# Performance work log

Hardware: AMD Instinct MI355X
Metric: run time of the kernel (lower is better)

Reference implementation:

```python
import jax, jax.numpy as jnp
import numpy as np

# Static configuration (matches init_kwargs)
B, C, H, W = 8, 64, 256, 256
WS = 8            # window size
HEADS = 4
DH = 16           # dim per head, HEADS*DH == C
L = WS * WS       # tokens per window
EPS_LN = 1e-5

# --- Swin relative-position index (static, numpy) ---
_coords = np.stack(np.meshgrid(np.arange(WS), np.arange(WS), indexing='ij'))  # [2,ws,ws]
_flat = _coords.reshape(2, -1)                                                # [2,L]
_rel = (_flat[:, :, None] - _flat[:, None, :]).transpose(1, 2, 0).copy()      # [L,L,2]
_rel[..., 0] += WS - 1
_rel[..., 1] += WS - 1
_rel[..., 0] *= 2 * WS - 1
REL_IDX = _rel.sum(-1)  # [L,L] ints in [0, (2ws-1)^2)


def _biasfree_ln(x, w):
    # x: [B,C,H,W]; BiasFree_LayerNorm over channel dim (biased var, no mean subtraction in scale)
    var = jnp.var(x, axis=1, keepdims=True)
    return x * jax.lax.rsqrt(var + EPS_LN) * w[None, :, None, None]


def _win_partition(t):  # [B,H,W,C] -> [N, L, C]
    t = t.reshape(B, H // WS, WS, W // WS, WS, C).transpose(0, 1, 3, 2, 4, 5)
    return t.reshape(-1, L, C)


def _win_reverse(t):  # [N, L, C] -> [B,H,W,C]
    t = t.reshape(B, H // WS, W // WS, WS, WS, C).transpose(0, 1, 3, 2, 4, 5)
    return t.reshape(B, H, W, C)


def _l2norm(t):
    # torch F.normalize(dim=-1) semantics
    n = jnp.sqrt(jnp.sum(t * t, axis=-1, keepdims=True))
    return t / jnp.maximum(n, 1e-12)


def _forward(x, illu_fea, ln1_w, ln2_w, w_qkv, b_qkv, rpb_table, w_proj, b_proj,
             temperature, w_qkv_m, w_dw, w_out_m):
    # ---------- spatial (window) attention branch ----------
    xs = _biasfree_ln(x, ln1_w).transpose(0, 2, 3, 1)          # [B,H,W,C]
    xw = _win_partition(xs)                                     # [N,L,C]
    iw = _win_partition(illu_fea.transpose(0, 2, 3, 1))         # [N,L,C]
    iw = iw.reshape(-1, L, HEADS, DH).transpose(0, 2, 1, 3)     # [N,h,L,d]

    qkv = (xw @ w_qkv + b_qkv).reshape(-1, L, 3, HEADS, DH).transpose(2, 0, 3, 1, 4)
    q, k, v = qkv[0], qkv[1], qkv[2]                            # [N,h,L,d]
    scale = DH ** (-0.5)
    attn = jnp.einsum('nhld,nhmd->nhlm', q * scale, k)          # [N,h,L,L]
    bias = rpb_table[REL_IDX.reshape(-1)].reshape(L, L, HEADS).transpose(2, 0, 1)
    attn = jax.nn.softmax(attn + bias[None], axis=-1)
    v = v * iw                                                  # illumination modulation
    out = jnp.einsum('nhlm,nhmd->nhld', attn, v)
    out = out.transpose(0, 2, 1, 3).reshape(-1, L, C) @ w_proj + b_proj
    win_out = _win_reverse(out).transpose(0, 3, 1, 2)           # [B,C,H,W]

    # ---------- channel (MDTA) attention branch ----------
    xm = _biasfree_ln(x, ln2_w)
    qkv_m = jnp.einsum('oc,bchw->bohw', w_qkv_m, xm)            # 1x1 conv, [B,3C,H,W]
    qkv_m = jax.lax.conv_general_dilated(
        qkv_m, w_dw, (1, 1), 'SAME', feature_group_count=3 * C,
        dimension_numbers=('NCHW', 'OIHW', 'NCHW'))             # depthwise 3x3
    qm, km, vm = jnp.split(qkv_m, 3, axis=1)                    # [B,C,H,W] each

    def heads(t):
        return t.reshape(B, HEADS, DH, H * W)                   # b (n d) h w -> b n d (hw)
    qm, km, vm, im = heads(qm), heads(km), heads(vm), heads(illu_fea)
    qm = _l2norm(qm)
    km = _l2norm(km)
    attn_c = jnp.einsum('bndx,bnex->bnde', qm, km) * temperature[None]  # [B,h,d,d]
    attn_c = jax.nn.softmax(attn_c, axis=-1)
    vm = vm * im                                                # illumination modulation
    out_c = jnp.einsum('bnde,bnex->bndx', attn_c, vm).reshape(B, C, H, W)
    mdta_out = jnp.einsum('oc,bchw->bohw', w_out_m, out_c)

    return x + win_out + mdta_out


def setup_inputs() -> dict:
    key = jax.random.key(0)
    ks = jax.random.split(key, 10)
    f32 = jnp.float32
    return {
        'x': jax.random.normal(ks[0], (B, C, H, W), f32),
        'illu_fea': jax.random.uniform(ks[1], (B, C, H, W), f32),
        'ln1_w': jnp.ones((C,), f32),
        'ln2_w': jnp.ones((C,), f32),
        'w_qkv': jax.random.normal(ks[2], (C, 3 * C), f32) * 0.02,
        'b_qkv': jnp.zeros((3 * C,), f32),
        'rpb_table': jax.random.normal(ks[3], ((2 * WS - 1) ** 2, HEADS), f32) * 0.02,
        'w_proj': jax.random.normal(ks[4], (C, C), f32) * 0.02,
        'b_proj': jnp.zeros((C,), f32),
        'temperature': jnp.ones((HEADS, 1, 1), f32),
        'w_qkv_m': jax.random.normal(ks[5], (3 * C, C), f32) * 0.02,
        'w_dw': jax.random.normal(ks[6], (3 * C, 1, 3, 3), f32) * 0.1,
        'w_out_m': jax.random.normal(ks[7], (C, C), f32) * 0.02,
    }


def reference(x, illu_fea, ln1_w, ln2_w, w_qkv, b_qkv, rpb_table, w_proj, b_proj,
              temperature, w_qkv_m, w_dw, w_out_m):
    return _forward(x, illu_fea, ln1_w, ln2_w, w_qkv, b_qkv, rpb_table, w_proj,
                    b_proj, temperature, w_qkv_m, w_dw, w_out_m)
```

## Files before the change

kernel.cpp:

```cpp
#include <hip/hip_runtime.h>
#include <hip/hip_bf16.h>

#define HW 65536
#define WIDTH 256
#define SP_OFF 77856768ull

typedef __attribute__((ext_vector_type(8))) short short8v;
typedef __attribute__((ext_vector_type(4))) short short4v;
typedef __attribute__((ext_vector_type(4))) float f32x4;

__device__ inline float bf2f(unsigned short u) {
  unsigned int i = ((unsigned int)u) << 16;
  float f; __builtin_memcpy(&f, &i, 4); return f;
}
__device__ inline unsigned short f2bf(float x) {
  __hip_bfloat16 h = __float2bfloat16(x);
  unsigned short u; __builtin_memcpy(&u, &h, 2); return u;
}

#define XH_IDX(p, g) ((p)*64 + ((((g) ^ ((p)&7)))<<3))
#define QC_IDX(ch, px) ((ch)*256 + ((((px)>>3) ^ ((ch)&7))<<3) + ((px)&7))
#define QCG_IDX(ch, G) ((ch)*256 + ((((G) ^ ((ch)&7)))<<3))

__global__ __launch_bounds__(256, 2) void k_spatial(
    const float* __restrict__ x, const float* __restrict__ illu,
    const float* __restrict__ ln1w, const float* __restrict__ wqkv,
    const float* __restrict__ bqkv, const float* __restrict__ rpb,
    const float* __restrict__ wproj, const float* __restrict__ bproj,
    float* __restrict__ out, unsigned short* __restrict__ sp, int use_sp)
{
  __shared__ __align__(16) unsigned short shbuf[9216];
  __shared__ __align__(16) unsigned short ks[64*72];
  __shared__ __align__(16) unsigned short vs[64*72];
  __shared__ __align__(16) unsigned short vsT[64*72];
  __shared__ __align__(16) unsigned short wq[192*72];
  __shared__ float rpbs[900];
  __shared__ float bq_s[192];
  __shared__ float rs_tok[64];

  unsigned short* xw = shbuf;
  unsigned short* qs = shbuf + 4608;

  const int tid = threadIdx.x;
  const int lb = ((blockIdx.x & 7) << 10) | (blockIdx.x >> 3);
  const int b = lb >> 10;
  const int win = lb & 1023;
  const int h0 = (win >> 5) << 3;
  const int w0 = (win & 31) << 3;
  const float* xb = x + (size_t)b * 64 * HW;

  const int lane = tid & 63;
  const int w = tid >> 6;
  const int fr = lane & 15;
  const int fg = lane >> 4;
  const int hb = w * 16;

  for (int i = tid; i < 900; i += 256) rpbs[i] = rpb[i];
  for (int i = tid; i < 192; i += 256) bq_s[i] = bqkv[i];
  for (int i = tid; i < 12288; i += 256) {
    int c = i / 192, o = i - c * 192;
    wq[o*72 + c] = f2bf(wqkv[i] * ln1w[c]);
  }
  for (int i = tid; i < 1024; i += 256) {
    int c = i >> 4, seg = i & 15;
    int row = seg >> 1, half = (seg & 1) * 4;
    float4 v4 = *(const float4*)&xb[(size_t)c * HW + (h0 + row) * WIDTH + w0 + half];
    int p = row * 8 + half;
    xw[(p+0)*72 + c] = f2bf(v4.x);
    xw[(p+1)*72 + c] = f2bf(v4.y);
    xw[(p+2)*72 + c] = f2bf(v4.z);
    xw[(p+3)*72 + c] = f2bf(v4.w);
  }
  __syncthreads();
  {
    int l = tid >> 2, q4 = tid & 3;
    short8v v8a = *(const short8v*)&xw[l*72 + q4*16];
    short8v v8b = *(const short8v*)&xw[l*72 + q4*16 + 8];
    float s = 0.f, s2 = 0.f;
    #pragma unroll
    for (int j = 0; j < 8; ++j) {
      float va = bf2f((unsigned short)v8a[j]), vb = bf2f((unsigned short)v8b[j]);
      s += va + vb; s2 += va * va + vb * vb;
    }
    s += __shfl_down(s, 1); s2 += __shfl_down(s2, 1);
    s += __shfl_down(s, 2); s2 += __shfl_down(s2, 2);
    if (q4 == 0) {
      float mean = s * 0.015625f;
      float var = s2 * 0.015625f - mean * mean;
      rs_tok[l] = rsqrtf(var + 1e-5f);
    }
  }
  __syncthreads();
  {
    short8v a[4][2];
    #pragma unroll
    for (int rt = 0; rt < 4; ++rt)
      #pragma unroll
      for (int kh = 0; kh < 2; ++kh)
        a[rt][kh] = *(const short8v*)&xw[(rt*16 + fr)*72 + kh*32 + fg*8];
    #pragma unroll
    for (int part = 0; part < 3; ++part) {
      int ob = part * 64 + hb;
      short8v b0 = *(const short8v*)&wq[(ob + fr)*72 + fg*8];
      short8v b1 = *(const short8v*)&wq[(ob + fr)*72 + 32 + fg*8];
      float bias = bq_s[ob + fr];
      #pragma unroll
      for (int rt = 0; rt < 4; ++rt) {
        f32x4 acc = {0.f, 0.f, 0.f, 0.f};
        acc = __builtin_amdgcn_mfma_f32_16x16x32_bf16(a[rt][0], b0, acc, 0, 0, 0);
        acc = __builtin_amdgcn_mfma_f32_16x16x32_bf16(a[rt][1], b1, acc, 0, 0, 0);
        #pragma unroll
        for (int r = 0; r < 4; ++r) {
          int t = rt*16 + fg*4 + r;
          float val = acc[r] * rs_tok[t] + bias;
          if (part == 0)      qs[t*72 + hb + fr] = f2bf(val * 0.25f);
          else if (part == 1) ks[t*72 + hb + fr] = f2bf(val);
          else                vs[t*72 + hb + fr] = f2bf(val);
        }
      }
    }
  }
  __syncthreads();
  {
    const float* ib = illu + (size_t)b * 64 * HW;
    for (int i = tid; i < 1024; i += 256) {
      int c = i >> 4, seg = i & 15;
      int row = seg >> 1, half = (seg & 1) * 4;
      float4 v4 = *(const float4*)&ib[(size_t)c * HW + (h0 + row) * WIDTH + w0 + half];
      int p = row * 8 + half;
      xw[(p+0)*72 + c] = f2bf(v4.x);
      xw[(p+1)*72 + c] = f2bf(v4.y);
      xw[(p+2)*72 + c] = f2bf(v4.z);
      xw[(p+3)*72 + c] = f2bf(v4.w);
    }
    for (int i = tid; i < 4096; i += 256) {
      int c = i >> 6, o = i & 63;
      wq[o*72 + c] = f2bf(wproj[i]);
    }
  }
  __syncthreads();
  for (int i = tid; i < 4096; i += 256) {
    int l = i >> 6, c = i & 63;
    unsigned short vb16 = f2bf(bf2f(vs[l*72 + c]) * bf2f(xw[l*72 + c]));
    vs[l*72 + c] = vb16;
    vsT[c*72 + ((((l >> 3) ^ (c & 7)) << 3) | (l & 7))] = vb16;
  }
  __syncthreads();
  float inv_s[4];
  {
    short8v zero8 = {0,0,0,0,0,0,0,0};
    short8v kf[4], qf[4];
    #pragma unroll
    for (int t = 0; t < 4; ++t) {
      if (fg < 2) {
        kf[t] = *(const short8v*)&ks[(t*16 + fr)*72 + hb + fg*8];
        qf[t] = *(const short8v*)&qs[(t*16 + fr)*72 + hb + fg*8];
      } else { kf[t] = zero8; qf[t] = zero8; }
    }
    f32x4 st[4][4];
    #pragma unroll
    for (int kt = 0; kt < 4; ++kt)
      #pragma unroll
      for (int qt = 0; qt < 4; ++qt) {
        f32x4 z = {0.f, 0.f, 0.f, 0.f};
        st[kt][qt] = __builtin_amdgcn_mfma_f32_16x16x32_bf16(kf[kt], qf[qt], z, 0, 0, 0);
      }
    float sc[4][16];
    #pragma unroll
    for (int qt = 0; qt < 4; ++qt) {
      int qi = qt*2 + (fr >> 3);
      int qj = fr & 7;
      float mx = -1e30f;
      #pragma unroll
      for (int kt = 0; kt < 4; ++kt) {
        int ki = kt*2 + (fg >> 1);
        int kj0 = (fg & 1) * 4;
        int base = ((qi - ki + 7)*15 + (qj - kj0 + 7))*4 + w;
        #pragma unroll
        for (int r = 0; r < 4; ++r) {
          float v = st[kt][qt][r] + rpbs[base - 4*r];
          sc[qt][kt*4 + r] = v;
          mx = fmaxf(mx, v);
        }
      }
      mx = fmaxf(mx, __shfl_xor(mx, 16));
      mx = fmaxf(mx, __shfl_xor(mx, 32));
      float ss = 0.f;
      #pragma unroll
      for (int j = 0; j < 16; ++j) { float e = __expf(sc[qt][j] - mx); sc[qt][j] = e; ss += e; }
      ss += __shfl_xor(ss, 16);
      ss += __shfl_xor(ss, 32);
      inv_s[qt] = 1.f / ss;
    }
    __syncthreads();
    unsigned short* pb = shbuf + w * 2304;
    f32x4 ot[4];
    #pragma unroll
    for (int nt = 0; nt < 4; ++nt) { f32x4 z = {0.f,0.f,0.f,0.f}; ot[nt] = z; }
    #pragma unroll
    for (int P = 0; P < 2; ++P) {
      #pragma unroll
      for (int qt = 0; qt < 4; ++qt)
        #pragma unroll
        for (int k2 = 0; k2 < 2; ++k2) {
          int kt = 2*P + k2;
          unsigned int lo = (unsigned)f2bf(sc[qt][kt*4+0]) | ((unsigned)f2bf(sc[qt][kt*4+1]) << 16);
          unsigned int hi = (unsigned)f2bf(sc[qt][kt*4+2]) | ((unsigned)f2bf(sc[qt][kt*4+3]) << 16);
          uint2 pk; pk.x = lo; pk.y = hi;
          *(uint2*)&pb[(qt*16 + fr)*36 + k2*16 + fg*4] = pk;
        }
      __syncthreads();
      short8v av = *(const short8v*)&vsT[(hb + fr)*72 + (((P*4 + fg) ^ ((hb + fr) & 7)) << 3)];
      #pragma unroll
      for (int nt = 0; nt < 4; ++nt) {
        short4v p0 = *(const short4v*)&pb[(nt*16 + fr)*36 + fg*8];
        short4v p1 = *(const short4v*)&pb[(nt*16 + fr)*36 + fg*8 + 4];
        short8v bv;
        #pragma unroll
        for (int j = 0; j < 4; ++j) { bv[j] = p0[j]; bv[4+j] = p1[j]; }
        ot[nt] = __builtin_amdgcn_mfma_f32_16x16x32_bf16(av, bv, ot[nt], 0, 0, 0);
      }
      __syncthreads();
    }
    #pragma unroll
    for (int nt = 0; nt < 4; ++nt) {
      float iv = inv_s[nt];
      unsigned int lo = (unsigned)f2bf(ot[nt][0]*iv) | ((unsigned)f2bf(ot[nt][1]*iv) << 16);
      unsigned int hi = (unsigned)f2bf(ot[nt][2]*iv) | ((unsigned)f2bf(ot[nt][3]*iv) << 16);
      uint2 pk; pk.x = lo; pk.y = hi;
      *(uint2*)&ks[(nt*16 + fr)*72 + hb + fg*4] = pk;
    }
  }
  __syncthreads();
  {
    short8v a[4][2];
    #pragma unroll
    for (int rt = 0; rt < 4; ++rt)
      #pragma unroll
      for (int kh = 0; kh < 2; ++kh)
        a[rt][kh] = *(const short8v*)&ks[(rt*16 + fr)*72 + kh*32 + fg*8];
    short8v b0 = *(const short8v*)&wq[(hb + fr)*72 + fg*8];
    short8v b1 = *(const short8v*)&wq[(hb + fr)*72 + 32 + fg*8];
    #pragma unroll
    for (int rt = 0; rt < 4; ++rt) {
      f32x4 acc = {0.f, 0.f, 0.f, 0.f};
      acc = __builtin_amdgcn_mfma_f32_16x16x32_bf16(a[rt][0], b0, acc, 0, 0, 0);
      acc = __builtin_amdgcn_mfma_f32_16x16x32_bf16(a[rt][1], b1, acc, 0, 0, 0);
      #pragma unroll
      for (int r = 0; r < 4; ++r)
        vs[(rt*16 + fg*4 + r)*72 + hb + fr] = f2bf(acc[r]);
    }
  }
  __syncthreads();
  if (use_sp) {
    unsigned short* spw = sp + (size_t)(b * 1024 + win) * 4096;
    for (int i = tid; i < 1024; i += 256) {
      int row = i >> 7, rem = i & 127;
      int c = rem >> 1, half = (rem & 1) * 4;
      int p = row * 8 + half;
      size_t gofs = (size_t)c * HW + (h0 + row) * WIDTH + w0 + half;
      float4 xr4 = *(const float4*)&xb[gofs];
      float bp = bproj[c];
      unsigned int lo = (unsigned)f2bf(xr4.x + bp + bf2f(vs[(p+0)*72 + c]))
                      | ((unsigned)f2bf(xr4.y + bp + bf2f(vs[(p+1)*72 + c])) << 16);
      unsigned int hi = (unsigned)f2bf(xr4.z + bp + bf2f(vs[(p+2)*72 + c]))
                      | ((unsigned)f2bf(xr4.w + bp + bf2f(vs[(p+3)*72 + c])) << 16);
      uint2 pk; pk.x = lo; pk.y = hi;
      *(uint2*)&spw[row*512 + c*8 + half] = pk;
    }
  } else {
    for (int i = tid; i < 1024; i += 256) {
      int o = i >> 4, seg = i & 15;
      int row = seg >> 1, half = (seg & 1) * 4;
      int p = row * 8 + half;
      size_t gofs = (size_t)o * HW + (h0 + row) * WIDTH + w0 + half;
      float4 xr4 = *(const float4*)&xb[gofs];
      float bp = bproj[o];
      float4 r;
      r.x = xr4.x + bp + bf2f(vs[(p+0)*72 + o]);
      r.y = xr4.y + bp + bf2f(vs[(p+1)*72 + o]);
      r.z = xr4.z + bp + bf2f(vs[(p+2)*72 + o]);
      r.w = xr4.w + bp + bf2f(vs[(p+3)*72 + o]);
      *(float4*)&out[(size_t)b * 64 * HW + gofs] = r;
    }
  }
}

__global__ __launch_bounds__(256, 2) void k_chan_qkv(
    const float* __restrict__ x, const float* __restrict__ illu,
    const float* __restrict__ ln2w, const float* __restrict__ w1,
    const float* __restrict__ wdw,
    unsigned short* __restrict__ vm, float* __restrict__ Gp,
    float* __restrict__ Nqp, float* __restrict__ Nkp)
{
  __shared__ __align__(16) unsigned short xh[336*64];
  __shared__ __align__(16) unsigned short tb[16*360];
  __shared__ __align__(16) unsigned short qc[16*256];
  __shared__ __align__(16) unsigned short kc[16*256];
  __shared__ float rsp[324];

  const int tid = threadIdx.x;
  const int blk = blockIdx.x;
  const int b = blk >> 8;
  const int tile = blk & 255;
  const int ty0 = (tile >> 4) << 4, tx0 = (tile & 15) << 4;
  const float* xb = x + (size_t)b * 64 * HW;

  for (int i = tid; i < 64 * 324; i += 256) {
    int c = i / 324, p = i - c * 324;
    int hy = p / 18, hx = p - hy * 18;
    int gy = ty0 + hy - 1, gx = tx0 + hx - 1;
    float v = 0.f;
    if (gy >= 0 && gy < 256 && gx >= 0 && gx < 256)
      v = xb[(size_t)c * HW + gy * WIDTH + gx];
    xh[XH_IDX(p, c >> 3) + (c & 7)] = f2bf(v);
  }
  for (int i = tid; i < 12 * 64; i += 256) {
    int p = 324 + (i >> 6), c = i & 63;
    xh[XH_IDX(p, c >> 3) + (c & 7)] = 0;
  }
  __syncthreads();
  for (int p = tid; p < 324; p += 256) {
    float s = 0.f, s2 = 0.f;
    #pragma unroll
    for (int g = 0; g < 8; ++g) {
      short8v v8 = *(const short8v*)&xh[XH_IDX(p, g)];
      #pragma unroll
      for (int j = 0; j < 8; ++j) { float v = bf2f((unsigned short)v8[j]); s += v; s2 += v * v; }
    }
    float mean = s * 0.015625f;
    float var = s2 * 0.015625f - mean * mean;
    rsp[p] = rsqrtf(var + 1e-5f);
  }
  __syncthreads();

  const int lane = tid & 63;
  const int wid = tid >> 6;
  const int fcol = lane & 15;
  const int fk = lane >> 4;
  const int dpy = (tid >> 2) & 15;
  const int dg = tid & 3;

  auto gemm_chunk = [&](int wbase) {
    short8v bf[2];
    const float* wr = w1 + (size_t)(wbase + fcol) * 64;
    #pragma unroll
    for (int s = 0; s < 2; ++s) {
      int cs = fk * 8 + s * 32;
      #pragma unroll
      for (int j = 0; j < 8; ++j)
        bf[s][j] = (short)f2bf(wr[cs + j] * ln2w[cs + j]);
    }
    for (int t = wid; t < 21; t += 4) {
      int ar = t * 16 + fcol;
      short8v a0 = *(const short8v*)&xh[XH_IDX(ar, fk)];
      short8v a1 = *(const short8v*)&xh[XH_IDX(ar, fk + 4)];
      f32x4 acc = {0.f, 0.f, 0.f, 0.f};
      acc = __builtin_amdgcn_mfma_f32_16x16x32_bf16(a0, bf[0], acc, 0, 0, 0);
      acc = __builtin_amdgcn_mfma_f32_16x16x32_bf16(a1, bf[1], acc, 0, 0, 0);
      #pragma unroll
      for (int r = 0; r < 4; ++r) {
        int px = t * 16 + fk * 4 + r;
        if (px < 324) {
          int hy = px / 18, hx = px - hy * 18;
          tb[fcol * 360 + hy * 20 + hx] = f2bf(acc[r] * rsp[px]);
        }
      }
    }
  };

  float dout4[4][4];
  auto dw_chunk = [&](int wbase) {
    #pragma unroll
    for (int oc4 = 0; oc4 < 4; ++oc4) {
      int oc = wid * 4 + oc4;
      const float* w9 = wdw + (size_t)(wbase + oc) * 9;
      float wk[9];
      #pragma unroll
      for (int t = 0; t < 9; ++t) wk[t] = w9[t];
      float a0 = 0.f, a1 = 0.f, a2 = 0.f, a3 = 0.f;
      #pragma unroll
      for (int ky = 0; ky < 3; ++ky) {
        int base = oc * 360 + (dpy + ky) * 20 + dg * 4;
        short4v t4 = *(const short4v*)&tb[base];
        unsigned int t2 = *(const unsigned int*)&tb[base + 4];
        float e0 = bf2f((unsigned short)t4[0]);
        float e1 = bf2f((unsigned short)t4[1]);
        float e2 = bf2f((unsigned short)t4[2]);
        float e3 = bf2f((unsigned short)t4[3]);
        float e4 = bf2f((unsigned short)(t2 & 0xffff));
        float e5 = bf2f((unsigned short)(t2 >> 16));
        float k0 = wk[ky*3+0], k1 = wk[ky*3+1], k2 = wk[ky*3+2];
        a0 += k0*e0 + k1*e1 + k2*e2;
        a1 += k0*e1 + k1*e2 + k2*e3;
        a2 += k0*e2 + k1*e3 + k2*e4;
        a3 += k0*e3 + k1*e4 + k2*e5;
      }
      dout4[oc4][0] = a0; dout4[oc4][1] = a1;
      dout4[oc4][2] = a2; dout4[oc4][3] = a3;
    }
  };

  for (int n = 0; n < 4; ++n) {
    gemm_chunk(16 * n);
    __syncthreads();
    dw_chunk(16 * n);
    #pragma unroll
    for (int oc4 = 0; oc4 < 4; ++oc4)
      #pragma unroll
      for (int i = 0; i < 4; ++i)
        qc[QC_IDX(wid*4 + oc4, dpy*16 + dg*4 + i)] = f2bf(dout4[oc4][i]);
    __syncthreads();
    {
      int ch = tid >> 4, seg = tid & 15;
      float s = 0.f;
      #pragma unroll
      for (int j = 0; j < 16; ++j) { float v = bf2f(qc[QC_IDX(ch, seg * 16 + j)]); s += v * v; }
      s += __shfl_xor(s, 1); s += __shfl_xor(s, 2); s += __shfl_xor(s, 4); s += __shfl_xor(s, 8);
      if (seg == 0) Nqp[(size_t)blk * 64 + n * 16 + ch] = s;
    }
    gemm_chunk(64 + 16 * n);
    __syncthreads();
    dw_chunk(64 + 16 * n);
    #pragma unroll
    for (int oc4 = 0; oc4 < 4; ++oc4)
      #pragma unroll
      for (int i = 0; i < 4; ++i)
        kc[QC_IDX(wid*4 + oc4, dpy*16 + dg*4 + i)] = f2bf(dout4[oc4][i]);
    __syncthreads();
    {
      int ch = tid >> 4, seg = tid & 15;
      float s = 0.f;
      #pragma unroll
      for (int j = 0; j < 16; ++j) { float v = bf2f(kc[QC_IDX(ch, seg * 16 + j)]); s += v * v; }
      s += __shfl_xor(s, 1); s += __shfl_xor(s, 2); s += __shfl_xor(s, 4); s += __shfl_xor(s, 8);
      if (seg == 0) Nkp[(size_t)blk * 64 + n * 16 + ch] = s;
    }
    if (wid == 0) {
      f32x4 g = {0.f, 0.f, 0.f, 0.f};
      #pragma unroll
      for (int s = 0; s < 8; ++s) {
        int G = fk + 4 * s;
        short8v aq = *(const short8v*)&qc[QCG_IDX(fcol, G)];
        short8v bk = *(const short8v*)&kc[QCG_IDX(fcol, G)];
        g = __builtin_amdgcn_mfma_f32_16x16x32_bf16(aq, bk, g, 0, 0, 0);
      }
      float* gp = Gp + ((size_t)blk * 4 + n) * 256;
      #pragma unroll
      for (int r = 0; r < 4; ++r) gp[(fk * 4 + r) * 16 + fcol] = g[r];
    }
  }
  const float* ib = illu + (size_t)b * 64 * HW;
  for (int j = 0; j < 4; ++j) {
    gemm_chunk(128 + 16 * j);
    __syncthreads();
    dw_chunk(128 + 16 * j);
    int gy = ty0 + dpy, gx = tx0 + dg * 4;
    size_t ppos = (size_t)gy * WIDTH + gx;
    #pragma unroll
    for (int oc4 = 0; oc4 < 4; ++oc4) {
      int vc = 16 * j + wid * 4 + oc4;
      float4 iv4 = *(const float4*)&ib[(size_t)vc * HW + ppos];
      unsigned int lo = (unsigned)f2bf(dout4[oc4][0] * iv4.x)
                      | ((unsigned)f2bf(dout4[oc4][1] * iv4.y) << 16);
      unsigned int hi = (unsigned)f2bf(dout4[oc4][2] * iv4.z)
                      | ((unsigned)f2bf(dout4[oc4][3] * iv4.w) << 16);
      uint2 pk; pk.x = lo; pk.y = hi;
      *(uint2*)&vm[((size_t)b * 64 + vc) * HW + ppos] = pk;
    }
    __syncthreads();
  }
}

__global__ __launch_bounds__(256) void k_reduce1(
    const float* __restrict__ Gp, const float* __restrict__ Nqp, const float* __restrict__ Nkp,
    float* __restrict__ G2, float* __restrict__ Nq2, float* __restrict__ Nk2)
{
  const int blk = blockIdx.x;
  const int b = blk >> 5, g = blk & 31;
  const int tid = threadIdx.x;
  float ga[4] = {0.f, 0.f, 0.f, 0.f};
  for (int t = 0; t < 8; ++t) {
    const float* src = Gp + ((size_t)(b * 256 + g * 8 + t)) * 1024;
    #pragma unroll
    for (int j = 0; j < 4; ++j) ga[j] += src[tid + j * 256];
  }
  float* dst = G2 + ((size_t)(b * 32 + g)) * 1024;
  #pragma unroll
  for (int j = 0; j < 4; ++j) dst[tid + j * 256] = ga[j];
  if (tid < 128) {
    int ch = tid & 63; bool isq = tid < 64;
    const float* np = isq ? Nqp : Nkp;
    float s = 0.f;
    for (int t = 0; t < 8; ++t) s += np[((size_t)(b * 256 + g * 8 + t)) * 64 + ch];
    (isq ? Nq2 : Nk2)[(size_t)(b * 32 + g) * 64 + ch] = s;
  }
}

__global__ __launch_bounds__(256) void k_reduce2(
    const float* __restrict__ G2, const float* __restrict__ Nq2, const float* __restrict__ Nk2,
    const float* __restrict__ temp, const float* __restrict__ wout, float* __restrict__ M)
{
  __shared__ float Gs[1024];
  __shared__ float As[4][16][17];
  __shared__ float nq[64], nk[64];
  const int b = blockIdx.x;
  const int tid = threadIdx.x;
  float ga[4] = {0.f, 0.f, 0.f, 0.f};
  for (int g = 0; g < 32; ++g) {
    const float* src = G2 + ((size_t)(b * 32 + g)) * 1024;
    #pragma unroll
    for (int j = 0; j < 4; ++j) ga[j] += src[tid + j * 256];
  }
  #pragma unroll
  for (int j = 0; j < 4; ++j) Gs[tid + j * 256] = ga[j];
  if (tid < 128) {
    int ch = tid & 63; bool isq = tid < 64;
    const float* n2 = isq ? Nq2 : Nk2;
    float s = 0.f;
    for (int g = 0; g < 32; ++g) s += n2[(size_t)(b * 32 + g) * 64 + ch];
    float r = fmaxf(sqrtf(s), 1e-12f);
    (isq ? nq : nk)[ch] = r;
  }
  __syncthreads();
  if (tid < 64) {
    int n = tid >> 4, d = tid & 15;
    float tv = temp[n];
    float row[16]; float mx = -1e30f;
    #pragma unroll
    for (int e = 0; e < 16; ++e) {
      float v = Gs[n * 256 + d * 16 + e] / (nq[n * 16 + d] * nk[n * 16 + e]) * tv;
      row[e] = v; mx = fmaxf(mx, v);
    }
    float s = 0.f;
    #pragma unroll
    for (int e = 0; e < 16; ++e) { float ev = __expf(row[e] - mx); row[e] = ev; s += ev; }
    float inv = 1.f / s;
    #pragma unroll
    for (int e = 0; e < 16; ++e) As[n][d][e] = row[e] * inv;
  }
  __syncthreads();
  float* Mb = M + (size_t)b * 4096;
  for (int i = tid; i < 4096; i += 256) {
    int o = i >> 6, cp = i & 63;
    int n = cp >> 4, e = cp & 15;
    float a = 0.f;
    #pragma unroll
    for (int d = 0; d < 16; ++d) a += wout[o * 64 + n * 16 + d] * As[n][d][e];
    Mb[i] = a;
  }
}

__global__ __launch_bounds__(256, 3) void k_mdta_out(
    const unsigned short* __restrict__ vm, const float* __restrict__ M,
    const unsigned short* __restrict__ sp, int use_sp,
    float* __restrict__ out)
{
  __shared__ __align__(16) float Ml[4096];
  __shared__ __align__(16) unsigned short spl[64 * 264];
  const int blk = blockIdx.x;
  const int b = blk >> 8;
  const int y = blk & 255;
  const int tid = threadIdx.x;

  const float* Mb = M + (size_t)b * 4096;
  for (int i = tid; i < 4096; i += 256) Ml[i] = Mb[i];
  if (use_sp) {
    int wy = y >> 3, py = y & 7;
    const unsigned short* spb = sp + ((((size_t)b * 1024 + wy * 32) * 8) + py) * 512;
    for (int k = 0; k < 8; ++k) {
      int i3 = k * 256 + tid;
      int o = i3 & 63, wx = i3 >> 6;
      short8v v8 = *(const short8v*)&spb[(size_t)wx * 4096 + o * 8];
      *(short8v*)&spl[o * 264 + wx * 8] = v8;
    }
  }
  __syncthreads();
  float xcol[64];
  const unsigned short* vb = vm + (size_t)b * 64 * HW + y * 256 + tid;
  #pragma unroll
  for (int c = 0; c < 64; ++c) xcol[c] = bf2f(vb[(size_t)c * HW]);
  float* ob = out + (size_t)b * 64 * HW + y * 256 + tid;
  for (int o = 0; o < 64; ++o) {
    const float4* mr = (const float4*)&Ml[o * 64];
    float acc = 0.f;
    #pragma unroll
    for (int g = 0; g < 16; ++g) {
      float4 m4 = mr[g];
      acc += m4.x * xcol[g*4] + m4.y * xcol[g*4+1] + m4.z * xcol[g*4+2] + m4.w * xcol[g*4+3];
    }
    if (use_sp) ob[(size_t)o * HW] = bf2f(spl[o * 264 + tid]) + acc;
    else        ob[(size_t)o * HW] += acc;
  }
}

extern "C" void kernel_launch(void* const* d_in, const int* in_sizes, int n_in,
                              void* d_out, int out_size, void* d_ws, size_t ws_size,
                              hipStream_t stream) {
  const float* x     = (const float*)d_in[0];
  const float* illu  = (const float*)d_in[1];
  const float* ln1w  = (const float*)d_in[2];
  const float* ln2w  = (const float*)d_in[3];
  const float* wqkv  = (const float*)d_in[4];
  const float* bqkv  = (const float*)d_in[5];
  const float* rpb   = (const float*)d_in[6];
  const float* wproj = (const float*)d_in[7];
  const float* bproj = (const float*)d_in[8];
  const float* temp  = (const float*)d_in[9];
  const float* w1    = (const float*)d_in[10];
  const float* wdw   = (const float*)d_in[11];
  const float* wout  = (const float*)d_in[12];
  float* out = (float*)d_out;

  char* ws = (char*)d_ws;
  unsigned short* vm = (unsigned short*)ws;
  float* Gp  = (float*)(ws + 67108864);
  float* Nqp = (float*)(ws + 75497472);
  float* Nkp = (float*)(ws + 76021760);
  float* G2  = (float*)(ws + 76546048);
  float* Nq2 = (float*)(ws + 77594624);
  float* Nk2 = (float*)(ws + 77660160);
  float* M   = (float*)(ws + 77725696);
  unsigned short* sp = (unsigned short*)(ws + SP_OFF);
  int use_sp = (ws_size >= SP_OFF + 67108864ull) ? 1 : 0;

  k_spatial<<<8192, 256, 0, stream>>>(x, illu, ln1w, wqkv, bqkv, rpb, wproj, bproj,
                                      out, sp, use_sp);
  k_chan_qkv<<<2048, 256, 0, stream>>>(x, illu, ln2w, w1, wdw, vm, Gp, Nqp, Nkp);
  k_reduce1<<<256, 256, 0, stream>>>(Gp, Nqp, Nkp, G2, Nq2, Nk2);
  k_reduce2<<<8, 256, 0, stream>>>(G2, Nq2, Nk2, temp, wout, M);
  k_mdta_out<<<2048, 256, 0, stream>>>(vm, M, sp, use_sp, out);
}
```

Before: 789.2 us.

## Persist spatial blocks over four windows and pair q/k chunks in channel kernel

```diff
diff --git a/kernel.cpp b/kernel.cpp
--- a/kernel.cpp
+++ b/kernel.cpp
@@ -22,7 +22,7 @@
 #define QC_IDX(ch, px) ((ch)*256 + ((((px)>>3) ^ ((ch)&7))<<3) + ((px)&7))
 #define QCG_IDX(ch, G) ((ch)*256 + ((((G) ^ ((ch)&7)))<<3))
 
-__global__ __launch_bounds__(256, 2) void k_spatial(
+__global__ __launch_bounds__(256, 3) void k_spatial(
     const float* __restrict__ x, const float* __restrict__ illu,
     const float* __restrict__ ln1w, const float* __restrict__ wqkv,
     const float* __restrict__ bqkv, const float* __restrict__ rpb,
@@ -33,21 +33,17 @@
   __shared__ __align__(16) unsigned short ks[64*72];
   __shared__ __align__(16) unsigned short vs[64*72];
   __shared__ __align__(16) unsigned short vsT[64*72];
-  __shared__ __align__(16) unsigned short wq[192*72];
   __shared__ float rpbs[900];
-  __shared__ float bq_s[192];
   __shared__ float rs_tok[64];
 
   unsigned short* xw = shbuf;
   unsigned short* qs = shbuf + 4608;
 
   const int tid = threadIdx.x;
-  const int lb = ((blockIdx.x & 7) << 10) | (blockIdx.x >> 3);
-  const int b = lb >> 10;
-  const int win = lb & 1023;
-  const int h0 = (win >> 5) << 3;
-  const int w0 = (win & 31) << 3;
+  const int b = blockIdx.x & 7;
+  const int grp = blockIdx.x >> 3;
   const float* xb = x + (size_t)b * 64 * HW;
+  const float* ib = illu + (size_t)b * 64 * HW;
 
   const int lane = tid & 63;
   const int w = tid >> 6;
@@ -56,73 +52,92 @@
   const int hb = w * 16;
 
   for (int i = tid; i < 900; i += 256) rpbs[i] = rpb[i];
-  for (int i = tid; i < 192; i += 256) bq_s[i] = bqkv[i];
-  for (int i = tid; i < 12288; i += 256) {
-    int c = i / 192, o = i - c * 192;
-    wq[o*72 + c] = f2bf(wqkv[i] * ln1w[c]);
-  }
-  for (int i = tid; i < 1024; i += 256) {
-    int c = i >> 4, seg = i & 15;
-    int row = seg >> 1, half = (seg & 1) * 4;
-    float4 v4 = *(const float4*)&xb[(size_t)c * HW + (h0 + row) * WIDTH + w0 + half];
-    int p = row * 8 + half;
-    xw[(p+0)*72 + c] = f2bf(v4.x);
-    xw[(p+1)*72 + c] = f2bf(v4.y);
-    xw[(p+2)*72 + c] = f2bf(v4.z);
-    xw[(p+3)*72 + c] = f2bf(v4.w);
-  }
-  __syncthreads();
-  {
-    int l = tid >> 2, q4 = tid & 3;
-    short8v v8a = *(const short8v*)&xw[l*72 + q4*16];
-    short8v v8b = *(const short8v*)&xw[l*72 + q4*16 + 8];
-    float s = 0.f, s2 = 0.f;
+
+  short8v bfq[3][2];
+  float biasr[3];
+  #pragma unroll
+  for (int part = 0; part < 3; ++part) {
+    int o = part * 64 + hb + fr;
+    biasr[part] = bqkv[o];
+    #pragma unroll
+    for (int kh = 0; kh < 2; ++kh)
+      #pragma unroll
+      for (int j = 0; j < 8; ++j) {
+        int c = kh * 32 + fg * 8 + j;
+        bfq[part][kh][j] = (short)f2bf(wqkv[c * 192 + o] * ln1w[c]);
+      }
+  }
+  short8v bfp[2];
+  #pragma unroll
+  for (int kh = 0; kh < 2; ++kh)
     #pragma unroll
     for (int j = 0; j < 8; ++j) {
-      float va = bf2f((unsigned short)v8a[j]), vb = bf2f((unsigned short)v8b[j]);
-      s += va + vb; s2 += va * va + vb * vb;
-    }
-    s += __shfl_down(s, 1); s2 += __shfl_down(s2, 1);
-    s += __shfl_down(s, 2); s2 += __shfl_down(s2, 2);
-    if (q4 == 0) {
-      float mean = s * 0.015625f;
-      float var = s2 * 0.015625f - mean * mean;
-      rs_tok[l] = rsqrtf(var + 1e-5f);
-    }
-  }
-  __syncthreads();
-  {
-    short8v a[4][2];
-    #pragma unroll
-    for (int rt = 0; rt < 4; ++rt)
-      #pragma unroll
-      for (int kh = 0; kh < 2; ++kh)
-        a[rt][kh] = *(const short8v*)&xw[(rt*16 + fr)*72 + kh*32 + fg*8];
-    #pragma unroll
-    for (int part = 0; part < 3; ++part) {
-      int ob = part * 64 + hb;
-      short8v b0 = *(const short8v*)&wq[(ob + fr)*72 + fg*8];
-      short8v b1 = *(const short8v*)&wq[(ob + fr)*72 + 32 + fg*8];
-      float bias = bq_s[ob + fr];
-      #pragma unroll
-      for (int rt = 0; rt < 4; ++rt) {
-        f32x4 acc = {0.f, 0.f, 0.f, 0.f};
-        acc = __builtin_amdgcn_mfma_f32_16x16x32_bf16(a[rt][0], b0, acc, 0, 0, 0);
-        acc = __builtin_amdgcn_mfma_f32_16x16x32_bf16(a[rt][1], b1, acc, 0, 0, 0);
-        #pragma unroll
-        for (int r = 0; r < 4; ++r) {
-          int t = rt*16 + fg*4 + r;
-          float val = acc[r] * rs_tok[t] + bias;
-          if (part == 0)      qs[t*72 + hb + fr] = f2bf(val * 0.25f);
-          else if (part == 1) ks[t*72 + hb + fr] = f2bf(val);
-          else                vs[t*72 + hb + fr] = f2bf(val);
+      int c = kh * 32 + fg * 8 + j;
+      bfp[kh][j] = (short)f2bf(wproj[c * 64 + hb + fr]);
+    }
+
+  for (int wi = 0; wi < 4; ++wi) {
+    const int win = (grp << 2) + wi;
+    const int h0 = (win >> 5) << 3;
+    const int w0 = (win & 31) << 3;
+
+    for (int i = tid; i < 1024; i += 256) {
+      int c = i >> 4, seg = i & 15;
+      int row = seg >> 1, half = (seg & 1) * 4;
+      float4 v4 = *(const float4*)&xb[(size_t)c * HW + (h0 + row) * WIDTH + w0 + half];
+      int p = row * 8 + half;
+      xw[(p+0)*72 + c] = f2bf(v4.x);
+      xw[(p+1)*72 + c] = f2bf(v4.y);
+      xw[(p+2)*72 + c] = f2bf(v4.z);
+      xw[(p+3)*72 + c] = f2bf(v4.w);
+    }
+    __syncthreads();
+    {
+      int l = tid >> 2, q4 = tid & 3;
+      short8v v8a = *(const short8v*)&xw[l*72 + q4*16];
+      short8v v8b = *(const short8v*)&xw[l*72 + q4*16 + 8];
+      float s = 0.f, s2 = 0.f;
+      #pragma unroll
+      for (int j = 0; j < 8; ++j) {
+        float va = bf2f((unsigned short)v8a[j]), vb = bf2f((unsigned short)v8b[j]);
+        s += va + vb; s2 += va * va + vb * vb;
+      }
+      s += __shfl_down(s, 1); s2 += __shfl_down(s2, 1);
+      s += __shfl_down(s, 2); s2 += __shfl_down(s2, 2);
+      if (q4 == 0) {
+        float mean = s * 0.015625f;
+        float var = s2 * 0.015625f - mean * mean;
+        rs_tok[l] = rsqrtf(var + 1e-5f);
+      }
+    }
+    __syncthreads();
+    {
+      short8v a[4][2];
+      #pragma unroll
+      for (int rt = 0; rt < 4; ++rt)
+        #pragma unroll
+        for (int kh = 0; kh < 2; ++kh)
+          a[rt][kh] = *(const short8v*)&xw[(rt*16 + fr)*72 + kh*32 + fg*8];
+      #pragma unroll
+      for (int part = 0; part < 3; ++part) {
+        float bias = biasr[part];
+        #pragma unroll
+        for (int rt = 0; rt < 4; ++rt) {
+          f32x4 acc = {0.f, 0.f, 0.f, 0.f};
+          acc = __builtin_amdgcn_mfma_f32_16x16x32_bf16(a[rt][0], bfq[part][0], acc, 0, 0, 0);
+          acc = __builtin_amdgcn_mfma_f32_16x16x32_bf16(a[rt][1], bfq[part][1], acc, 0, 0, 0);
+          #pragma unroll
+          for (int r = 0; r < 4; ++r) {
+            int t = rt*16 + fg*4 + r;
+            float val = acc[r] * rs_tok[t] + bias;
+            if (part == 0)      qs[t*72 + hb + fr] = f2bf(val * 0.25f);
+            else if (part == 1) ks[t*72 + hb + fr] = f2bf(val);
+            else                vs[t*72 + hb + fr] = f2bf(val);
+          }
         }
       }
     }
-  }
-  __syncthreads();
-  {
-    const float* ib = illu + (size_t)b * 64 * HW;
+    __syncthreads();
     for (int i = tid; i < 1024; i += 256) {
       int c = i >> 4, seg = i & 15;
       int row = seg >> 1, half = (seg & 1) * 4;
@@ -133,156 +148,151 @@
       xw[(p+2)*72 + c] = f2bf(v4.z);
       xw[(p+3)*72 + c] = f2bf(v4.w);
     }
+    __syncthreads();
     for (int i = tid; i < 4096; i += 256) {
-      int c = i >> 6, o = i & 63;
-      wq[o*72 + c] = f2bf(wproj[i]);
-    }
-  }
-  __syncthreads();
-  for (int i = tid; i < 4096; i += 256) {
-    int l = i >> 6, c = i & 63;
-    unsigned short vb16 = f2bf(bf2f(vs[l*72 + c]) * bf2f(xw[l*72 + c]));
-    vs[l*72 + c] = vb16;
-    vsT[c*72 + ((((l >> 3) ^ (c & 7)) << 3) | (l & 7))] = vb16;
-  }
-  __syncthreads();
-  float inv_s[4];
-  {
-    short8v zero8 = {0,0,0,0,0,0,0,0};
-    short8v kf[4], qf[4];
-    #pragma unroll
-    for (int t = 0; t < 4; ++t) {
-      if (fg < 2) {
-        kf[t] = *(const short8v*)&ks[(t*16 + fr)*72 + hb + fg*8];
-        qf[t] = *(const short8v*)&qs[(t*16 + fr)*72 + hb + fg*8];
-      } else { kf[t] = zero8; qf[t] = zero8; }
-    }
-    f32x4 st[4][4];
-    #pragma unroll
-    for (int kt = 0; kt < 4; ++kt)
+      int l = i >> 6, c = i & 63;
+      unsigned short vb16 = f2bf(bf2f(vs[l*72 + c]) * bf2f(xw[l*72 + c]));
+      vs[l*72 + c] = vb16;
+      vsT[c*72 + ((((l >> 3) ^ (c & 7)) << 3) | (l & 7))] = vb16;
+    }
+    __syncthreads();
+    float inv_s[4];
+    {
+      short8v zero8 = {0,0,0,0,0,0,0,0};
+      short8v kf[4], qf[4];
+      #pragma unroll
+      for (int t = 0; t < 4; ++t) {
+        if (fg < 2) {
+          kf[t] = *(const short8v*)&ks[(t*16 + fr)*72 + hb + fg*8];
+          qf[t] = *(const short8v*)&qs[(t*16 + fr)*72 + hb + fg*8];
+        } else { kf[t] = zero8; qf[t] = zero8; }
+      }
+      f32x4 st[4][4];
+      #pragma unroll
+      for (int kt = 0; kt < 4; ++kt)
+        #pragma unroll
+        for (int qt = 0; qt < 4; ++qt) {
+          f32x4 z = {0.f, 0.f, 0.f, 0.f};
+          st[kt][qt] = __builtin_amdgcn_mfma_f32_16x16x32_bf16(kf[kt], qf[qt], z, 0, 0, 0);
+        }
+      float sc[4][16];
       #pragma unroll
       for (int qt = 0; qt < 4; ++qt) {
-        f32x4 z = {0.f, 0.f, 0.f, 0.f};
-        st[kt][qt] = __builtin_amdgcn_mfma_f32_16x16x32_bf16(kf[kt], qf[qt], z, 0, 0, 0);
-      }
-    float sc[4][16];
-    #pragma unroll
-    for (int qt = 0; qt < 4; ++qt) {
-      int qi = qt*2 + (fr >> 3);
-      int qj = fr & 7;
-      float mx = -1e30f;
-      #pragma unroll
-      for (int kt = 0; kt < 4; ++kt) {
-        int ki = kt*2 + (fg >> 1);
-        int kj0 = (fg & 1) * 4;
-        int base = ((qi - ki + 7)*15 + (qj - kj0 + 7))*4 + w;
-        #pragma unroll
-        for (int r = 0; r < 4; ++r) {
-          float v = st[kt][qt][r] + rpbs[base - 4*r];
-          sc[qt][kt*4 + r] = v;
-          mx = fmaxf(mx, v);
+        int qi = qt*2 + (fr >> 3);
+        int qj = fr & 7;
+        float mx = -1e30f;
+        #pragma unroll
+        for (int kt = 0; kt < 4; ++kt) {
+          int ki = kt*2 + (fg >> 1);
+          int kj0 = (fg & 1) * 4;
+          int base = ((qi - ki + 7)*15 + (qj - kj0 + 7))*4 + w;
+          #pragma unroll
+          for (int r = 0; r < 4; ++r) {
+            float v = st[kt][qt][r] + rpbs[base - 4*r];
+            sc[qt][kt*4 + r] = v;
+            mx = fmaxf(mx, v);
+          }
         }
-      }
-      mx = fmaxf(mx, __shfl_xor(mx, 16));
-      mx = fmaxf(mx, __shfl_xor(mx, 32));
-      float ss = 0.f;
-      #pragma unroll
-      for (int j = 0; j < 16; ++j) { float e = __expf(sc[qt][j] - mx); sc[qt][j] = e; ss += e; }
-      ss += __shfl_xor(ss, 16);
-      ss += __shfl_xor(ss, 32);
-      inv_s[qt] = 1.f / ss;
-    }
-    __syncthreads();
-    unsigned short* pb = shbuf + w * 2304;
-    f32x4 ot[4];
-    #pragma unroll
-    for (int nt = 0; nt < 4; ++nt) { f32x4 z = {0.f,0.f,0.f,0.f}; ot[nt] = z; }
-    #pragma unroll
-    for (int P = 0; P < 2; ++P) {
-      #pragma unroll
-      for (int qt = 0; qt < 4; ++qt)
-        #pragma unroll
-        for (int k2 = 0; k2 < 2; ++k2) {
-          int kt = 2*P + k2;
-          unsigned int lo = (unsigned)f2bf(sc[qt][kt*4+0]) | ((unsigned)f2bf(sc[qt][kt*4+1]) << 16);
-          unsigned int hi = (unsigned)f2bf(sc[qt][kt*4+2]) | ((unsigned)f2bf(sc[qt][kt*4+3]) << 16);
-          uint2 pk; pk.x = lo; pk.y = hi;
-          *(uint2*)&pb[(qt*16 + fr)*36 + k2*16 + fg*4] = pk;
+        mx = fmaxf(mx, __shfl_xor(mx, 16));
+        mx = fmaxf(mx, __shfl_xor(mx, 32));
+        float ss = 0.f;
+        #pragma unroll
+        for (int j = 0; j < 16; ++j) { float e = __expf(sc[qt][j] - mx); sc[qt][j] = e; ss += e; }
+        ss += __shfl_xor(ss, 16);
+        ss += __shfl_xor(ss, 32);
+        inv_s[qt] = 1.f / ss;
+      }
+      __syncthreads();
+      unsigned short* pb = shbuf + w * 2304;
+      f32x4 ot[4];
+      #pragma unroll
+      for (int nt = 0; nt < 4; ++nt) { f32x4 z = {0.f,0.f,0.f,0.f}; ot[nt] = z; }
+      #pragma unroll
+      for (int P = 0; P < 2; ++P) {
+        #pragma unroll
+        for (int qt = 0; qt < 4; ++qt)
+          #pragma unroll
+          for (int k2 = 0; k2 < 2; ++k2) {
+            int kt = 2*P + k2;
+            unsigned int lo = (unsigned)f2bf(sc[qt][kt*4+0]) | ((unsigned)f2bf(sc[qt][kt*4+1]) << 16);
+            unsigned int hi = (unsigned)f2bf(sc[qt][kt*4+2]) | ((unsigned)f2bf(sc[qt][kt*4+3]) << 16);
+            uint2 pk; pk.x = lo; pk.y = hi;
+            *(uint2*)&pb[(qt*16 + fr)*36 + k2*16 + fg*4] = pk;
+          }
+        __syncthreads();
+        short8v av = *(const short8v*)&vsT[(hb + fr)*72 + (((P*4 + fg) ^ ((hb + fr) & 7)) << 3)];
+        #pragma unroll
+        for (int nt = 0; nt < 4; ++nt) {
+          short4v p0 = *(const short4v*)&pb[(nt*16 + fr)*36 + fg*8];
+          short4v p1 = *(const short4v*)&pb[(nt*16 + fr)*36 + fg*8 + 4];
+          short8v bv;
+          #pragma unroll
+          for (int j = 0; j < 4; ++j) { bv[j] = p0[j]; bv[4+j] = p1[j]; }
+          ot[nt] = __builtin_amdgcn_mfma_f32_16x16x32_bf16(av, bv, ot[nt], 0, 0, 0);
         }
-      __syncthreads();
-      short8v av = *(const short8v*)&vsT[(hb + fr)*72 + (((P*4 + fg) ^ ((hb + fr) & 7)) << 3)];
+        __syncthreads();
+      }
       #pragma unroll
       for (int nt = 0; nt < 4; ++nt) {
-        short4v p0 = *(const short4v*)&pb[(nt*16 + fr)*36 + fg*8];
-        short4v p1 = *(const short4v*)&pb[(nt*16 + fr)*36 + fg*8 + 4];
-        short8v bv;
-        #pragma unroll
-        for (int j = 0; j < 4; ++j) { bv[j] = p0[j]; bv[4+j] = p1[j]; }
-        ot[nt] = __builtin_amdgcn_mfma_f32_16x16x32_bf16(av, bv, ot[nt], 0, 0, 0);
-      }
-      __syncthreads();
-    }
-    #pragma unroll
-    for (int nt = 0; nt < 4; ++nt) {
-      float iv = inv_s[nt];
-      unsigned int lo = (unsigned)f2bf(ot[nt][0]*iv) | ((unsigned)f2bf(ot[nt][1]*iv) << 16);
-      unsigned int hi = (unsigned)f2bf(ot[nt][2]*iv) | ((unsigned)f2bf(ot[nt][3]*iv) << 16);
-      uint2 pk; pk.x = lo; pk.y = hi;
-      *(uint2*)&ks[(nt*16 + fr)*72 + hb + fg*4] = pk;
-    }
-  }
-  __syncthreads();
-  {
-    short8v a[4][2];
-    #pragma unroll
-    for (int rt = 0; rt < 4; ++rt)
-      #pragma unroll
-      for (int kh = 0; kh < 2; ++kh)
-        a[rt][kh] = *(const short8v*)&ks[(rt*16 + fr)*72 + kh*32 + fg*8];
-    short8v b0 = *(const short8v*)&wq[(hb + fr)*72 + fg*8];
-    short8v b1 = *(const short8v*)&wq[(hb + fr)*72 + 32 + fg*8];
-    #pragma unroll
-    for (int rt = 0; rt < 4; ++rt) {
-      f32x4 acc = {0.f, 0.f, 0.f, 0.f};
-      acc = __builtin_amdgcn_mfma_f32_16x16x32_bf16(a[rt][0], b0, acc, 0, 0, 0);
-      acc = __builtin_amdgcn_mfma_f32_16x16x32_bf16(a[rt][1], b1, acc, 0, 0, 0);
-      #pragma unroll
-      for (int r = 0; r < 4; ++r)
-        vs[(rt*16 + fg*4 + r)*72 + hb + fr] = f2bf(acc[r]);
-    }
-  }
-  __syncthreads();
-  if (use_sp) {
-    unsigned short* spw = sp + (size_t)(b * 1024 + win) * 4096;
-    for (int i = tid; i < 1024; i += 256) {
-      int row = i >> 7, rem = i & 127;
-      int c = rem >> 1, half = (rem & 1) * 4;
-      int p = row * 8 + half;
-      size_t gofs = (size_t)c * HW + (h0 + row) * WIDTH + w0 + half;
-      float4 xr4 = *(const float4*)&xb[gofs];
-      float bp = bproj[c];
-      unsigned int lo = (unsigned)f2bf(xr4.x + bp + bf2f(vs[(p+0)*72 + c]))
-                      | ((unsigned)f2bf(xr4.y + bp + bf2f(vs[(p+1)*72 + c])) << 16);
-      unsigned int hi = (unsigned)f2bf(xr4.z + bp + bf2f(vs[(p+2)*72 + c]))
-                      | ((unsigned)f2bf(xr4.w + bp + bf2f(vs[(p+3)*72 + c])) << 16);
-      uint2 pk; pk.x = lo; pk.y = hi;
-      *(uint2*)&spw[row*512 + c*8 + half] = pk;
-    }
-  } else {
-    for (int i = tid; i < 1024; i += 256) {
-      int o = i >> 4, seg = i & 15;
-      int row = seg >> 1, half = (seg & 1) * 4;
-      int p = row * 8 + half;
-      size_t gofs = (size_t)o * HW + (h0 + row) * WIDTH + w0 + half;
-      float4 xr4 = *(const float4*)&xb[gofs];
-      float bp = bproj[o];
-      float4 r;
-      r.x = xr4.x + bp + bf2f(vs[(p+0)*72 + o]);
-      r.y = xr4.y + bp + bf2f(vs[(p+1)*72 + o]);
-      r.z = xr4.z + bp + bf2f(vs[(p+2)*72 + o]);
-      r.w = xr4.w + bp + bf2f(vs[(p+3)*72 + o]);
-      *(float4*)&out[(size_t)b * 64 * HW + gofs] = r;
-    }
+        float iv = inv_s[nt];
+        unsigned int lo = (unsigned)f2bf(ot[nt][0]*iv) | ((unsigned)f2bf(ot[nt][1]*iv) << 16);
+        unsigned int hi = (unsigned)f2bf(ot[nt][2]*iv) | ((unsigned)f2bf(ot[nt][3]*iv) << 16);
+        uint2 pk; pk.x = lo; pk.y = hi;
+        *(uint2*)&ks[(nt*16 + fr)*72 + hb + fg*4] = pk;
+      }
+    }
+    __syncthreads();
+    {
+      short8v a[4][2];
+      #pragma unroll
+      for (int rt = 0; rt < 4; ++rt)
+        #pragma unroll
+        for (int kh = 0; kh < 2; ++kh)
+          a[rt][kh] = *(const short8v*)&ks[(rt*16 + fr)*72 + kh*32 + fg*8];
+      #pragma unroll
+      for (int rt = 0; rt < 4; ++rt) {
+        f32x4 acc = {0.f, 0.f, 0.f, 0.f};
+        acc = __builtin_amdgcn_mfma_f32_16x16x32_bf16(a[rt][0], bfp[0], acc, 0, 0, 0);
+        acc = __builtin_amdgcn_mfma_f32_16x16x32_bf16(a[rt][1], bfp[1], acc, 0, 0, 0);
+        #pragma unroll
+        for (int r = 0; r < 4; ++r)
+          vs[(rt*16 + fg*4 + r)*72 + hb + fr] = f2bf(acc[r]);
+      }
+    }
+    __syncthreads();
+    if (use_sp) {
+      unsigned short* spw = sp + (size_t)(b * 1024 + win) * 4096;
+      for (int i = tid; i < 1024; i += 256) {
+        int row = i >> 7, rem = i & 127;
+        int c = rem >> 1, half = (rem & 1) * 4;
+        int p = row * 8 + half;
+        size_t gofs = (size_t)c * HW + (h0 + row) * WIDTH + w0 + half;
+        float4 xr4 = *(const float4*)&xb[gofs];
+        float bp = bproj[c];
+        unsigned int lo = (unsigned)f2bf(xr4.x + bp + bf2f(vs[(p+0)*72 + c]))
+                        | ((unsigned)f2bf(xr4.y + bp + bf2f(vs[(p+1)*72 + c])) << 16);
+        unsigned int hi = (unsigned)f2bf(xr4.z + bp + bf2f(vs[(p+2)*72 + c]))
+                        | ((unsigned)f2bf(xr4.w + bp + bf2f(vs[(p+3)*72 + c])) << 16);
+        uint2 pk; pk.x = lo; pk.y = hi;
+        *(uint2*)&spw[row*512 + c*8 + half] = pk;
+      }
+    } else {
+      for (int i = tid; i < 1024; i += 256) {
+        int o = i >> 4, seg = i & 15;
+        int row = seg >> 1, half = (seg & 1) * 4;
+        int p = row * 8 + half;
+        size_t gofs = (size_t)o * HW + (h0 + row) * WIDTH + w0 + half;
+        float4 xr4 = *(const float4*)&xb[gofs];
+        float bp = bproj[o];
+        float4 r;
+        r.x = xr4.x + bp + bf2f(vs[(p+0)*72 + o]);
+        r.y = xr4.y + bp + bf2f(vs[(p+1)*72 + o]);
+        r.z = xr4.z + bp + bf2f(vs[(p+2)*72 + o]);
+        r.w = xr4.w + bp + bf2f(vs[(p+3)*72 + o]);
+        *(float4*)&out[(size_t)b * 64 * HW + gofs] = r;
+      }
+    }
+    __syncthreads();
   }
 }
 
@@ -293,11 +303,12 @@
     unsigned short* __restrict__ vm, float* __restrict__ Gp,
     float* __restrict__ Nqp, float* __restrict__ Nkp)
 {
-  __shared__ __align__(16) unsigned short xh[336*64];
-  __shared__ __align__(16) unsigned short tb[16*360];
+  __shared__ __align__(16) unsigned short xh[324*64];
+  __shared__ __align__(16) unsigned short tb[32*360];
   __shared__ __align__(16) unsigned short qc[16*256];
   __shared__ __align__(16) unsigned short kc[16*256];
-  __shared__ float rsp[324];
+
+  float* rsp = (float*)tb;
 
   const int tid = threadIdx.x;
   const int blk = blockIdx.x;
@@ -315,10 +326,6 @@
       v = xb[(size_t)c * HW + gy * WIDTH + gx];
     xh[XH_IDX(p, c >> 3) + (c & 7)] = f2bf(v);
   }
-  for (int i = tid; i < 12 * 64; i += 256) {
-    int p = 324 + (i >> 6), c = i & 63;
-    xh[XH_IDX(p, c >> 3) + (c & 7)] = 0;
-  }
   __syncthreads();
   for (int p = tid; p < 324; p += 256) {
     float s = 0.f, s2 = 0.f;
@@ -331,6 +338,15 @@
     float mean = s * 0.015625f;
     float var = s2 * 0.015625f - mean * mean;
     rsp[p] = rsqrtf(var + 1e-5f);
+  }
+  __syncthreads();
+  for (int i = tid; i < 2592; i += 256) {
+    int p = i >> 3;
+    float rs = rsp[p];
+    short8v v8 = *(const short8v*)&xh[i * 8];
+    #pragma unroll
+    for (int j = 0; j < 8; ++j) v8[j] = (short)f2bf(bf2f((unsigned short)v8[j]) * rs);
+    *(short8v*)&xh[i * 8] = v8;
   }
   __syncthreads();
 
@@ -341,40 +357,49 @@
   const int dpy = (tid >> 2) & 15;
   const int dg = tid & 3;
 
-  auto gemm_chunk = [&](int wbase) {
-    short8v bf[2];
-    const float* wr = w1 + (size_t)(wbase + fcol) * 64;
+  auto gemm32 = [&](int qb, int kb) {
+    short8v bq[2], bk[2];
+    const float* wrq = w1 + (size_t)(qb + fcol) * 64;
+    const float* wrk = w1 + (size_t)(kb + fcol) * 64;
     #pragma unroll
     for (int s = 0; s < 2; ++s) {
       int cs = fk * 8 + s * 32;
       #pragma unroll
-      for (int j = 0; j < 8; ++j)
-        bf[s][j] = (short)f2bf(wr[cs + j] * ln2w[cs + j]);
+      for (int j = 0; j < 8; ++j) {
+        float lw = ln2w[cs + j];
+        bq[s][j] = (short)f2bf(wrq[cs + j] * lw);
+        bk[s][j] = (short)f2bf(wrk[cs + j] * lw);
+      }
     }
     for (int t = wid; t < 21; t += 4) {
       int ar = t * 16 + fcol;
       short8v a0 = *(const short8v*)&xh[XH_IDX(ar, fk)];
       short8v a1 = *(const short8v*)&xh[XH_IDX(ar, fk + 4)];
-      f32x4 acc = {0.f, 0.f, 0.f, 0.f};
-      acc = __builtin_amdgcn_mfma_f32_16x16x32_bf16(a0, bf[0], acc, 0, 0, 0);
-      acc = __builtin_amdgcn_mfma_f32_16x16x32_bf16(a1, bf[1], acc, 0, 0, 0);
+      f32x4 aq = {0.f, 0.f, 0.f, 0.f};
+      f32x4 ak = {0.f, 0.f, 0.f, 0.f};
+      aq = __builtin_amdgcn_mfma_f32_16x16x32_bf16(a0, bq[0], aq, 0, 0, 0);
+      aq = __builtin_amdgcn_mfma_f32_16x16x32_bf16(a1, bq[1], aq, 0, 0, 0);
+      ak = __builtin_amdgcn_mfma_f32_16x16x32_bf16(a0, bk[0], ak, 0, 0, 0);
+      ak = __builtin_amdgcn_mfma_f32_16x16x32_bf16(a1, bk[1], ak, 0, 0, 0);
       #pragma unroll
       for (int r = 0; r < 4; ++r) {
         int px = t * 16 + fk * 4 + r;
         if (px < 324) {
           int hy = px / 18, hx = px - hy * 18;
-          tb[fcol * 360 + hy * 20 + hx] = f2bf(acc[r] * rsp[px]);
+          tb[fcol * 360 + hy * 20 + hx]        = f2bf(aq[r]);
+          tb[(16 + fcol) * 360 + hy * 20 + hx] = f2bf(ak[r]);
         }
       }
     }
   };
 
-  float dout4[4][4];
-  auto dw_chunk = [&](int wbase) {
-    #pragma unroll
-    for (int oc4 = 0; oc4 < 4; ++oc4) {
-      int oc = wid * 4 + oc4;
-      const float* w9 = wdw + (size_t)(wbase + oc) * 9;
+  float dout8[8][4];
+  auto dw32 = [&](int qwb, int kwb) {
+    #pragma unroll
+    for (int oc8 = 0; oc8 < 8; ++oc8) {
+      int oc = wid * 8 + oc8;
+      int ch = (oc < 16) ? (qwb + oc) : (kwb + oc - 16);
+      const float* w9 = wdw + (size_t)ch * 9;
       float wk[9];
       #pragma unroll
       for (int t = 0; t < 9; ++t) wk[t] = w9[t];
@@ -396,45 +421,39 @@
         a2 += k0*e2 + k1*e3 + k2*e4;
         a3 += k0*e3 + k1*e4 + k2*e5;
       }
-      dout4[oc4][0] = a0; dout4[oc4][1] = a1;
-      dout4[oc4][2] = a2; dout4[oc4][3] = a3;
+      dout8[oc8][0] = a0; dout8[oc8][1] = a1;
+      dout8[oc8][2] = a2; dout8[oc8][3] = a3;
     }
   };
 
   for (int n = 0; n < 4; ++n) {
-    gemm_chunk(16 * n);
-    __syncthreads();
-    dw_chunk(16 * n);
-    #pragma unroll
-    for (int oc4 = 0; oc4 < 4; ++oc4)
+    gemm32(16 * n, 64 + 16 * n);
+    __syncthreads();
+    dw32(16 * n, 64 + 16 * n);
+    #pragma unroll
+    for (int oc8 = 0; oc8 < 8; ++oc8) {
+      int oc = wid * 8 + oc8;
+      unsigned short* dst = (oc < 16) ? qc : kc;
+      int row = oc & 15;
       #pragma unroll
       for (int i = 0; i < 4; ++i)
-        qc[QC_IDX(wid*4 + oc4, dpy*16 + dg*4 + i)] = f2bf(dout4[oc4][i]);
+        dst[QC_IDX(row, dpy*16 + dg*4 + i)] = f2bf(dout8[oc8][i]);
+    }
     __syncthreads();
     {
       int ch = tid >> 4, seg = tid & 15;
-      float s = 0.f;
-      #pragma unroll
-      for (int j = 0; j < 16; ++j) { float v = bf2f(qc[QC_IDX(ch, seg * 16 + j)]); s += v * v; }
-      s += __shfl_xor(s, 1); s += __shfl_xor(s, 2); s += __shfl_xor(s, 4); s += __shfl_xor(s, 8);
-      if (seg == 0) Nqp[(size_t)blk * 64 + n * 16 + ch] = s;
-    }
-    gemm_chunk(64 + 16 * n);
-    __syncthreads();
-    dw_chunk(64 + 16 * n);
-    #pragma unroll
-    for (int oc4 = 0; oc4 < 4; ++oc4)
-      #pragma unroll
-      for (int i = 0; i < 4; ++i)
-        kc[QC_IDX(wid*4 + oc4, dpy*16 + dg*4 + i)] = f2bf(dout4[oc4][i]);
-    __syncthreads();
-    {
-      int ch = tid >> 4, seg = tid & 15;
-      float s = 0.f;
-      #pragma unroll
-      for (int j = 0; j < 16; ++j) { float v = bf2f(kc[QC_IDX(ch, seg * 16 + j)]); s += v * v; }
-      s += __shfl_xor(s, 1); s += __shfl_xor(s, 2); s += __shfl_xor(s, 4); s += __shfl_xor(s, 8);
-      if (seg == 0) Nkp[(size_t)blk * 64 + n * 16 + ch] = s;
+      float sq = 0.f, sk = 0.f;
+      #pragma unroll
+      for (int j = 0; j < 16; ++j) {
+        float vq = bf2f(qc[QC_IDX(ch, seg * 16 + j)]); sq += vq * vq;
+        float vk = bf2f(kc[QC_IDX(ch, seg * 16 + j)]); sk += vk * vk;
+      }
+      sq += __shfl_xor(sq, 1); sq += __shfl_xor(sq, 2); sq += __shfl_xor(sq, 4); sq += __shfl_xor(sq, 8);
+      sk += __shfl_xor(sk, 1); sk += __shfl_xor(sk, 2); sk += __shfl_xor(sk, 4); sk += __shfl_xor(sk, 8);
+      if (seg == 0) {
+        Nqp[(size_t)blk * 64 + n * 16 + ch] = sq;
+        Nkp[(size_t)blk * 64 + n * 16 + ch] = sk;
+      }
     }
     if (wid == 0) {
       f32x4 g = {0.f, 0.f, 0.f, 0.f};
@@ -451,20 +470,20 @@
     }
   }
   const float* ib = illu + (size_t)b * 64 * HW;
-  for (int j = 0; j < 4; ++j) {
-    gemm_chunk(128 + 16 * j);
-    __syncthreads();
-    dw_chunk(128 + 16 * j);
+  for (int j = 0; j < 2; ++j) {
+    gemm32(128 + 32 * j, 144 + 32 * j);
+    __syncthreads();
+    dw32(128 + 32 * j, 144 + 32 * j);
     int gy = ty0 + dpy, gx = tx0 + dg * 4;
     size_t ppos = (size_t)gy * WIDTH + gx;
     #pragma unroll
-    for (int oc4 = 0; oc4 < 4; ++oc4) {
-      int vc = 16 * j + wid * 4 + oc4;
+    for (int oc8 = 0; oc8 < 8; ++oc8) {
+      int vc = 32 * j + wid * 8 + oc8;
       float4 iv4 = *(const float4*)&ib[(size_t)vc * HW + ppos];
-      unsigned int lo = (unsigned)f2bf(dout4[oc4][0] * iv4.x)
-                      | ((unsigned)f2bf(dout4[oc4][1] * iv4.y) << 16);
-      unsigned int hi = (unsigned)f2bf(dout4[oc4][2] * iv4.z)
-                      | ((unsigned)f2bf(dout4[oc4][3] * iv4.w) << 16);
+      unsigned int lo = (unsigned)f2bf(dout8[oc8][0] * iv4.x)
+                      | ((unsigned)f2bf(dout8[oc8][1] * iv4.y) << 16);
+      unsigned int hi = (unsigned)f2bf(dout8[oc8][2] * iv4.z)
+                      | ((unsigned)f2bf(dout8[oc8][3] * iv4.w) << 16);
       uint2 pk; pk.x = lo; pk.y = hi;
       *(uint2*)&vm[((size_t)b * 64 + vc) * HW + ppos] = pk;
     }
@@ -624,7 +643,7 @@
   unsigned short* sp = (unsigned short*)(ws + SP_OFF);
   int use_sp = (ws_size >= SP_OFF + 67108864ull) ? 1 : 0;
 
-  k_spatial<<<8192, 256, 0, stream>>>(x, illu, ln1w, wqkv, bqkv, rpb, wproj, bproj,
+  k_spatial<<<2048, 256, 0, stream>>>(x, illu, ln1w, wqkv, bqkv, rpb, wproj, bproj,
                                       out, sp, use_sp);
   k_chan_qkv<<<2048, 256, 0, stream>>>(x, illu, ln2w, w1, wdw, vm, Gp, Nqp, Nkp);
   k_reduce1<<<256, 256, 0, stream>>>(Gp, Nqp, Nkp, G2, Nq2, Nk2);
```

Result: faster. 728.0 us (-7.7%).
